# Kernel optimization log

Measured on AMD Instinct MI355X. Metric: run time of the kernel, lower is better.

## Reference

```python
import jax, jax.numpy as jnp
import numpy as np

B_SZ, SEQ, D_MODEL, N_STATE = 4, 2048, 768, 16


def setup_inputs() -> dict:
    key = jax.random.key(0)
    ks = jax.random.split(key, 8)
    s = 1.0 / np.sqrt(D_MODEL)
    x = jax.random.normal(ks[0], (B_SZ, SEQ, D_MODEL), dtype=jnp.float32)
    W1 = jax.random.uniform(ks[1], (D_MODEL, D_MODEL), jnp.float32, -s, s)
    b1 = jax.random.uniform(ks[2], (D_MODEL,), jnp.float32, -s, s)
    W2 = jax.random.uniform(ks[3], (D_MODEL, N_STATE), jnp.float32, -s, s)
    b2 = jax.random.uniform(ks[4], (N_STATE,), jnp.float32, -s, s)
    W3 = jax.random.uniform(ks[5], (D_MODEL, N_STATE), jnp.float32, -s, s)
    b3 = jax.random.uniform(ks[6], (N_STATE,), jnp.float32, -s, s)
    # A: xavier_uniform over (d_model, state_size)
    a_bound = np.sqrt(6.0 / (D_MODEL + N_STATE))
    A = jax.random.uniform(ks[7], (D_MODEL, N_STATE), jnp.float32, -a_bound, a_bound)
    return {"x": x, "W1": W1, "b1": b1, "W2": W2, "b2": b2, "W3": W3, "b3": b3, "A": A}


def reference(x, W1, b1, W2, b2, W3, b3, A):
    # Input-dependent projections
    Bm = x @ W2 + b2                     # [b, l, n]
    Cm = x @ W3 + b3                     # [b, l, n]
    delta = jax.nn.softplus(x @ W1 + b1)  # [b, l, d]
    # Discretization (S6)
    dB = delta[..., None] * Bm[:, :, None, :]                 # [b, l, d, n]
    dA = jnp.exp(jnp.einsum('bld,dn->bldn', delta, A))        # [b, l, d, n]
    # Source initializes h to zeros, so the dA*h term vanishes (no recurrence).
    h0 = jnp.zeros_like(dB)
    h = dA * h0 + x[..., None] * dB                            # [b, l, d, n]
    y = jnp.einsum('bln,bldn->bld', Cm, h)                     # [b, l, d]
    return y
```

## Files before the change

kernel.cpp:

```cpp
#include <hip/hip_runtime.h>
#include <hip/hip_bf16.h>
#include <math.h>


#define M_ROWS 8192
#define DM 768
#define NS 16

typedef short bf16x8 __attribute__((ext_vector_type(8)));
typedef float f32x4 __attribute__((ext_vector_type(4)));

__device__ __forceinline__ unsigned short f2bf(float f) {
    union { float f; unsigned u; } v; v.f = f;
    unsigned r = v.u + 0x7FFF + ((v.u >> 16) & 1);
    return (unsigned short)(r >> 16);
}
__device__ __forceinline__ float bf2f(unsigned short h) {
    union { unsigned u; float f; } v; v.u = ((unsigned)h) << 16; return v.f;
}
__device__ __forceinline__ void async16(const void* g, void* l) {
    __builtin_amdgcn_global_load_lds(
        (const __attribute__((address_space(1))) void*)g,
        (__attribute__((address_space(3))) void*)l,
        16, 0, 0);
}
__device__ __forceinline__ float softplus_fast(float v) {
    return fmaxf(v, 0.f) + __logf(1.f + __expf(-fabsf(v)));
}

__global__ __launch_bounds__(256) void prep_kernel(
    const float* __restrict__ x,
    const float* __restrict__ W1,
    const float* __restrict__ W2,
    const float* __restrict__ W3,
    unsigned short* __restrict__ xb,
    unsigned short* __restrict__ w1t,
    unsigned short* __restrict__ w23t)
{
    __shared__ float tile[32][33];
    const int bid = blockIdx.x;
    const int tid = threadIdx.x;
    if (bid < 32) {
        const int n = bid, i = n >> 1;
        const float* src = (n & 1) ? W3 : W2;
        #pragma unroll
        for (int e = 0; e < 3; ++e) {
            int k = e * 256 + tid;
            w23t[n * DM + k] = f2bf(src[k * NS + i]);
        }
    } else if (bid < 608) {
        const int b2i = bid - 32;
        const int n0 = (b2i % 24) * 32, k0 = (b2i / 24) * 32;
        const int tx = tid & 31, ty = tid >> 5;
        #pragma unroll
        for (int i = 0; i < 4; ++i) {
            int k = ty + i * 8;
            tile[k][tx] = W1[(k0 + k) * DM + n0 + tx];
        }
        __syncthreads();
        #pragma unroll
        for (int i = 0; i < 4; ++i) {
            int n = ty + i * 8;
            w1t[(n0 + n) * DM + k0 + tx] = f2bf(tile[tx][n]);
        }
    } else {
        int i = (bid - 608) * 256 + tid;
        float4 v = ((const float4*)x)[i];
        ushort4 o;
        o.x = f2bf(v.x); o.y = f2bf(v.y); o.z = f2bf(v.z); o.w = f2bf(v.w);
        ((ushort4*)xb)[i] = o;
    }
}

__global__ __launch_bounds__(256) void gemm_fused_kernel(
    const unsigned short* __restrict__ xb,
    const unsigned short* __restrict__ w1t,
    const unsigned short* __restrict__ w23t,
    const float* __restrict__ b1,
    const float* __restrict__ b2, const float* __restrict__ b3,
    float* __restrict__ y)
{
    __shared__ __align__(16) char smem[29696];
    unsigned short* Al    = (unsigned short*)(smem);
    unsigned short* Bl    = (unsigned short*)(smem + 16384);
    unsigned short* Wl    = (unsigned short*)(smem + 24576);
    float*          spart = (float*)(smem + 28672);
    float*          ytile = (float*)(smem + 16384);

    const int b = blockIdx.x;
    const int c = b & 7, j = b >> 3;
    const int m0 = (c * 8 + j / 12) * 128;
    const int n0 = (j % 12) * 64;
    const int tid  = threadIdx.x;
    const int lane = tid & 63;
    const int wave = tid >> 6;
    const int wm = wave >> 1, wn = wave & 1;
    const int l15 = lane & 15, quad = lane >> 4;

    f32x4 acc[4][2];
    f32x4 accP[4];
    #pragma unroll
    for (int i = 0; i < 4; ++i) {
        accP[i] = (f32x4){0.f, 0.f, 0.f, 0.f};
        #pragma unroll
        for (int jj = 0; jj < 2; ++jj)
            acc[i][jj] = (f32x4){0.f, 0.f, 0.f, 0.f};
    }

    for (int k0 = 0; k0 < DM; k0 += 64) {
        #pragma unroll
        for (int i = 0; i < 4; ++i) {
            int ch = tid + i * 256;
            int r = ch >> 3, jg = (ch & 7) ^ (r & 7);
            async16(xb + (m0 + r) * DM + k0 + jg * 8, Al + ch * 8);
        }
        #pragma unroll
        for (int i = 0; i < 2; ++i) {
            int ch = tid + i * 256;
            int r = ch >> 3, jg = (ch & 7) ^ (r & 7);
            async16(w1t + (n0 + r) * DM + k0 + jg * 8, Bl + ch * 8);
        }
        {
            int ch = tid;
            int r = ch >> 3, jg = (ch & 7) ^ (r & 7);
            async16(w23t + r * DM + k0 + jg * 8, Wl + ch * 8);
        }
        __syncthreads();

        #pragma unroll
        for (int kk = 0; kk < 2; ++kk) {
            bf16x8 bfr[2], wfr;
            #pragma unroll
            for (int jj = 0; jj < 2; ++jj) {
                int rb = wn * 32 + jj * 16 + l15;
                int jb = (kk * 4 + quad) ^ (rb & 7);
                bfr[jj] = *(const bf16x8*)(Bl + rb * 64 + jb * 8);
            }
            {
                int rw = wn * 16 + l15;
                int jw = (kk * 4 + quad) ^ (rw & 7);
                wfr = *(const bf16x8*)(Wl + rw * 64 + jw * 8);
            }
            #pragma unroll
            for (int i = 0; i < 4; ++i) {
                int rr = wm * 64 + i * 16 + l15;
                int ja = (kk * 4 + quad) ^ (rr & 7);
                bf16x8 af = *(const bf16x8*)(Al + rr * 64 + ja * 8);
                #pragma unroll
                for (int jj = 0; jj < 2; ++jj)
                    acc[i][jj] = __builtin_amdgcn_mfma_f32_16x16x32_bf16(
                        af, bfr[jj], acc[i][jj], 0, 0, 0);
                accP[i] = __builtin_amdgcn_mfma_f32_16x16x32_bf16(
                    af, wfr, accP[i], 0, 0, 0);
            }
        }
        __syncthreads();
    }

    {
        const int p = wn * 8 + (l15 >> 1);
        const float bB = b2[p], bC = b3[p];
        #pragma unroll
        for (int i = 0; i < 4; ++i) {
            float sacc[4];
            #pragma unroll
            for (int r = 0; r < 4; ++r) {
                float v = accP[i][r];
                float pv = __shfl_xor(v, 1, 64);
                sacc[r] = (l15 & 1) ? (pv + bB) * (v + bC)
                                    : (v + bB) * (pv + bC);
                sacc[r] += __shfl_xor(sacc[r], 1, 64);
                sacc[r] += __shfl_xor(sacc[r], 2, 64);
                sacc[r] += __shfl_xor(sacc[r], 4, 64);
                sacc[r] += __shfl_xor(sacc[r], 8, 64);
            }
            if (l15 == 0) {
                #pragma unroll
                for (int r = 0; r < 4; ++r)
                    spart[wn * 128 + wm * 64 + i * 16 + quad * 4 + r] = 0.5f * sacc[r];
            }
        }
    }
    __syncthreads();

    const int row_l = tid >> 3;
    const int cg    = tid & 7;
    const int grow_base = m0 + (row_l >> 4) * 64 + (row_l & 15);
    const int gcol_r    = n0 + cg * 8;
    #pragma unroll
    for (int i = 0; i < 4; ++i) {
        const int rl = wm * 64 + i * 16 + quad * 4;
        float sv4[4];
        #pragma unroll
        for (int r = 0; r < 4; ++r)
            sv4[r] = spart[rl + r] + spart[128 + rl + r];
        #pragma unroll
        for (int jj = 0; jj < 2; ++jj) {
            const int tc = wn * 32 + jj * 16 + l15;
            const float bias = b1[n0 + tc];
            #pragma unroll
            for (int r = 0; r < 4; ++r) {
                float v = acc[i][jj][r] + bias;
                float sp = softplus_fast(v);
                ytile[(wm * 16 + quad * 4 + r) * 64 + tc] = sp * sv4[r];
            }
        }
        __syncthreads();
        const int grow = grow_base + i * 16;
        f32x4 t0 = *(const f32x4*)&ytile[row_l * 64 + cg * 8];
        f32x4 t1 = *(const f32x4*)&ytile[row_l * 64 + cg * 8 + 4];
        bf16x8 xv8 = *(const bf16x8*)(xb + grow * DM + gcol_r);
        f32x4 o0, o1;
        #pragma unroll
        for (int e = 0; e < 4; ++e) {
            o0[e] = t0[e] * bf2f((unsigned short)xv8[e]);
            o1[e] = t1[e] * bf2f((unsigned short)xv8[e + 4]);
        }
        *(f32x4*)(y + grow * DM + gcol_r)     = o0;
        *(f32x4*)(y + grow * DM + gcol_r + 4) = o1;
        if (i < 3) __syncthreads();
    }
}

extern "C" void kernel_launch(void* const* d_in, const int* in_sizes, int n_in,
                              void* d_out, int out_size, void* d_ws, size_t ws_size,
                              hipStream_t stream) {
    const float* x  = (const float*)d_in[0];
    const float* W1 = (const float*)d_in[1];
    const float* b1 = (const float*)d_in[2];
    const float* W2 = (const float*)d_in[3];
    const float* b2 = (const float*)d_in[4];
    const float* W3 = (const float*)d_in[5];
    const float* b3 = (const float*)d_in[6];
    float* y = (float*)d_out;

    unsigned short* xb   = (unsigned short*)d_ws;
    unsigned short* w1t  = (unsigned short*)((char*)d_ws + 12582912);
    unsigned short* w23t = (unsigned short*)((char*)d_ws + 13762560);

    prep_kernel<<<6752, 256, 0, stream>>>(x, W1, W2, W3, xb, w1t, w23t);
    gemm_fused_kernel<<<768, 256, 0, stream>>>(xb, w1t, w23t, b1, b2, b3, y);
}
```

Measured before the change: 114.8 us.

## Fuse x fp32-to-bf16 conversion into GEMM, loading fp32 x tiles directly

Drops the separate pass that converts x to bf16 in the prep kernel. The GEMM now streams fp32 x tiles into LDS with a swizzled layout and converts them to bf16 in registers right before the MFMA, and the epilogue multiplies by the original fp32 x. This removes a full write and reread of a bf16 copy of x, but doubles the LDS footprint and global traffic for the A tile, and repeats the conversion for every N-tile block (12 times per row).

```diff
diff --git a/kernel.cpp b/kernel.cpp
--- a/kernel.cpp
+++ b/kernel.cpp
@@ -8,15 +8,13 @@
 #define NS 16
 
 typedef short bf16x8 __attribute__((ext_vector_type(8)));
+typedef unsigned short u16x8 __attribute__((ext_vector_type(8)));
 typedef float f32x4 __attribute__((ext_vector_type(4)));
 
 __device__ __forceinline__ unsigned short f2bf(float f) {
     union { float f; unsigned u; } v; v.f = f;
     unsigned r = v.u + 0x7FFF + ((v.u >> 16) & 1);
     return (unsigned short)(r >> 16);
-}
-__device__ __forceinline__ float bf2f(unsigned short h) {
-    union { unsigned u; float f; } v; v.u = ((unsigned)h) << 16; return v.f;
 }
 __device__ __forceinline__ void async16(const void* g, void* l) {
     __builtin_amdgcn_global_load_lds(
@@ -29,11 +27,9 @@
 }
 
 __global__ __launch_bounds__(256) void prep_kernel(
-    const float* __restrict__ x,
     const float* __restrict__ W1,
     const float* __restrict__ W2,
     const float* __restrict__ W3,
-    unsigned short* __restrict__ xb,
     unsigned short* __restrict__ w1t,
     unsigned short* __restrict__ w23t)
 {
@@ -48,7 +44,7 @@
             int k = e * 256 + tid;
             w23t[n * DM + k] = f2bf(src[k * NS + i]);
         }
-    } else if (bid < 608) {
+    } else {
         const int b2i = bid - 32;
         const int n0 = (b2i % 24) * 32, k0 = (b2i / 24) * 32;
         const int tx = tid & 31, ty = tid >> 5;
@@ -63,29 +59,23 @@
             int n = ty + i * 8;
             w1t[(n0 + n) * DM + k0 + tx] = f2bf(tile[tx][n]);
         }
-    } else {
-        int i = (bid - 608) * 256 + tid;
-        float4 v = ((const float4*)x)[i];
-        ushort4 o;
-        o.x = f2bf(v.x); o.y = f2bf(v.y); o.z = f2bf(v.z); o.w = f2bf(v.w);
-        ((ushort4*)xb)[i] = o;
     }
 }
 
 __global__ __launch_bounds__(256) void gemm_fused_kernel(
-    const unsigned short* __restrict__ xb,
+    const float* __restrict__ x,
     const unsigned short* __restrict__ w1t,
     const unsigned short* __restrict__ w23t,
     const float* __restrict__ b1,
     const float* __restrict__ b2, const float* __restrict__ b3,
     float* __restrict__ y)
 {
-    __shared__ __align__(16) char smem[29696];
-    unsigned short* Al    = (unsigned short*)(smem);
-    unsigned short* Bl    = (unsigned short*)(smem + 16384);
-    unsigned short* Wl    = (unsigned short*)(smem + 24576);
-    float*          spart = (float*)(smem + 28672);
-    float*          ytile = (float*)(smem + 16384);
+    __shared__ __align__(16) char smem[46080];
+    float*          Alf   = (float*)(smem);
+    unsigned short* Bl    = (unsigned short*)(smem + 32768);
+    unsigned short* Wl    = (unsigned short*)(smem + 40960);
+    float*          spart = (float*)(smem + 45056);
+    float*          ytile = (float*)(smem);
 
     const int b = blockIdx.x;
     const int c = b & 7, j = b >> 3;
@@ -109,10 +99,11 @@
 
     for (int k0 = 0; k0 < DM; k0 += 64) {
         #pragma unroll
-        for (int i = 0; i < 4; ++i) {
+        for (int i = 0; i < 8; ++i) {
             int ch = tid + i * 256;
-            int r = ch >> 3, jg = (ch & 7) ^ (r & 7);
-            async16(xb + (m0 + r) * DM + k0 + jg * 8, Al + ch * 8);
+            int r = ch >> 4, cgs = ch & 15;
+            int u16i = (((cgs >> 1) ^ (r & 7)) << 1) | (cgs & 1);
+            async16(x + (m0 + r) * DM + k0 + u16i * 4, (char*)Alf + ch * 16);
         }
         #pragma unroll
         for (int i = 0; i < 2; ++i) {
@@ -144,8 +135,16 @@
             #pragma unroll
             for (int i = 0; i < 4; ++i) {
                 int rr = wm * 64 + i * 16 + l15;
-                int ja = (kk * 4 + quad) ^ (rr & 7);
-                bf16x8 af = *(const bf16x8*)(Al + rr * 64 + ja * 8);
+                int kp = kk * 4 + quad;
+                int p  = kp ^ (rr & 7);
+                const f32x4* ap = (const f32x4*)(Alf + rr * 64 + p * 8);
+                f32x4 a0 = ap[0], a1 = ap[1];
+                union { u16x8 h; bf16x8 v; } au;
+                au.h[0] = f2bf(a0[0]); au.h[1] = f2bf(a0[1]);
+                au.h[2] = f2bf(a0[2]); au.h[3] = f2bf(a0[3]);
+                au.h[4] = f2bf(a1[0]); au.h[5] = f2bf(a1[1]);
+                au.h[6] = f2bf(a1[2]); au.h[7] = f2bf(a1[3]);
+                bf16x8 af = au.v;
                 #pragma unroll
                 for (int jj = 0; jj < 2; ++jj)
                     acc[i][jj] = __builtin_amdgcn_mfma_f32_16x16x32_bf16(
@@ -209,12 +208,13 @@
         const int grow = grow_base + i * 16;
         f32x4 t0 = *(const f32x4*)&ytile[row_l * 64 + cg * 8];
         f32x4 t1 = *(const f32x4*)&ytile[row_l * 64 + cg * 8 + 4];
-        bf16x8 xv8 = *(const bf16x8*)(xb + grow * DM + gcol_r);
+        f32x4 xv0 = *(const f32x4*)(x + grow * DM + gcol_r);
+        f32x4 xv1 = *(const f32x4*)(x + grow * DM + gcol_r + 4);
         f32x4 o0, o1;
         #pragma unroll
         for (int e = 0; e < 4; ++e) {
-            o0[e] = t0[e] * bf2f((unsigned short)xv8[e]);
-            o1[e] = t1[e] * bf2f((unsigned short)xv8[e + 4]);
+            o0[e] = t0[e] * xv0[e];
+            o1[e] = t1[e] * xv1[e];
         }
         *(f32x4*)(y + grow * DM + gcol_r)     = o0;
         *(f32x4*)(y + grow * DM + gcol_r + 4) = o1;
@@ -234,10 +234,9 @@
     const float* b3 = (const float*)d_in[6];
     float* y = (float*)d_out;
 
-    unsigned short* xb   = (unsigned short*)d_ws;
-    unsigned short* w1t  = (unsigned short*)((char*)d_ws + 12582912);
-    unsigned short* w23t = (unsigned short*)((char*)d_ws + 13762560);
-
-    prep_kernel<<<6752, 256, 0, stream>>>(x, W1, W2, W3, xb, w1t, w23t);
-    gemm_fused_kernel<<<768, 256, 0, stream>>>(xb, w1t, w23t, b1, b2, b3, y);
-}
+    unsigned short* w1t  = (unsigned short*)d_ws;
+    unsigned short* w23t = (unsigned short*)((char*)d_ws + 1179648);
+
+    prep_kernel<<<608, 256, 0, stream>>>(W1, W2, W3, w1t, w23t);
+    gemm_fused_kernel<<<768, 256, 0, stream>>>(x, w1t, w23t, b1, b2, b3, y);
+}
```

After: 121.7 us. 6.0% more time.
